# Optimization experiments

Hardware: AMD Instinct MI355X
Metric: run time of the kernel (lower is better)

The kernel has to match this reference:

```python
import jax, jax.numpy as jnp
import numpy as np

B, OBS, TASK = 65536, 512, 128
D, M, N = 64, 32, 4  # embedding dim, module width, modules per layer


def setup_inputs() -> dict:
    key = jax.random.key(0)
    ks = jax.random.split(key, 16)

    def w(k, shape):
        fan_in = shape[-2]
        return jax.random.normal(k, shape, jnp.float32) * np.float32(np.sqrt(2.0 / fan_in))

    z = lambda *s: jnp.zeros(s, jnp.float32)
    return dict(
        obs=jax.random.normal(ks[0], (B, OBS), jnp.float32),
        task=jax.random.normal(ks[1], (B, TASK), jnp.float32),
        Ws1=w(ks[2], (OBS, D)), bs1=z(D),
        Ws2=w(ks[3], (D, D)), bs2=z(D),
        Wt=w(ks[4], (TASK, D)), bt=z(D),
        Wa0=w(ks[5], (D, N * N)), ba0=z(N * N),
        Wa1=w(ks[6], (D, N * N)), ba1=z(N * N),
        Wc0=w(ks[7], (N * N, D)), bc0=z(D),
        Wc1=w(ks[8], (2 * N * N, D)), bc1=z(D),
        We0=w(ks[9], (N, D, M)), be0=z(N, M),
        We1=w(ks[10], (N, M, M)), be1=z(N, M),
        We2=w(ks[11], (N, M, M)), be2=z(N, M),
    )


def reference(obs, task, Ws1, bs1, Ws2, bs2, Wt, bt, Wa0, ba0, Wa1, ba1,
              Wc0, bc0, Wc1, bc1, We0, be0, We1, be1, We2, be2):
    relu = jax.nn.relu
    # base encoders
    s = relu(relu(obs @ Ws1 + bs1) @ Ws2 + bs2)          # [B, D]
    t = relu(task @ Wt + bt)                              # [B, D]
    r0 = s * t                                            # first routing inputs [B, D]
    prev = jnp.broadcast_to(s[None], (N,) + s.shape)      # [N, B, D] (state emb fed to all layer-0 modules)

    # routing layer 0 -> 1
    a0 = jax.nn.softmax((r0 @ Wa0 + ba0).reshape(-1, N, N), axis=-1)   # [B, N_next, N_prev]
    m = relu(jnp.einsum('nbi,nio->nbo', prev, We0) + be0[:, None, :])  # [N, B, M] expert outputs
    prev = jnp.einsum('bij,jbd->ibd', a0, m)                           # [N, B, M] attention-combined
    r = relu((a0.reshape(-1, N * N) @ Wc0 + bc0) * r0)                 # updated routing inputs

    # routing layer 1 -> 2
    a1 = jax.nn.softmax((r @ Wa1 + ba1).reshape(-1, N, N), axis=-1)
    m = relu(jnp.einsum('nbi,nio->nbo', prev, We1) + be1[:, None, :])
    prev = jnp.einsum('bij,jbd->ibd', a1, m)
    attn_cat = jnp.concatenate([a0.reshape(-1, N * N), a1.reshape(-1, N * N)], axis=-1)
    r = relu((attn_cat @ Wc1 + bc1) * r0)  # computed as in original (unused afterward)

    # final module layer, plain sum over modules
    m = relu(jnp.einsum('nbi,nio->nbo', prev, We2) + be2[:, None, :])  # [N, B, M]
    return relu(m.sum(axis=0))                                          # [B, M]
```

## Files before the change

### kernel.cpp

```cpp
#include <hip/hip_runtime.h>
#include <hip/hip_bf16.h>


using f32x4 = __attribute__((ext_vector_type(4))) float;
using h16x4 = __attribute__((ext_vector_type(4))) _Float16;
using h16x8 = __attribute__((ext_vector_type(8))) _Float16;
using u32x4 = __attribute__((ext_vector_type(4))) unsigned int;
using u32x2 = __attribute__((ext_vector_type(2))) unsigned int;

#define MFMA16(a, b, c) __builtin_amdgcn_mfma_f32_16x16x16f16((a), (b), (c), 0, 0, 0)

__device__ __forceinline__ short h_bits(float f) {
  _Float16 h = (_Float16)f;
  return __builtin_bit_cast(short, h);
}

__device__ __forceinline__ void dma16(const void* g, char* l) {
  __builtin_amdgcn_global_load_lds(
      (const __attribute__((address_space(1))) unsigned int*)g,
      (__attribute__((address_space(3))) unsigned int*)l, 16, 0, 0);
}

__global__ void sm_convert_v12(
    const float* __restrict__ Ws1, const float* __restrict__ Ws2, const float* __restrict__ Wt,
    const float* __restrict__ Wa0, const float* __restrict__ Wa1, const float* __restrict__ Wc0,
    const float* __restrict__ We0, const float* __restrict__ We1, const float* __restrict__ We2,
    const float* __restrict__ bs1, const float* __restrict__ bs2, const float* __restrict__ bt,
    const float* __restrict__ ba0, const float* __restrict__ ba1, const float* __restrict__ bc0,
    const float* __restrict__ be0, const float* __restrict__ be1, const float* __restrict__ be2,
    short* __restrict__ wsh, float* __restrict__ biasf) {
  int d = blockIdx.x * 256 + threadIdx.x;
  if (d < 64512) {
    float v;
    if (d < 32768) {
      int kk   = d & 3;
      int ntip = (d >> 2) & 1;
      int p    = (d >> 3) & 15;
      int q    = (d >> 7) & 3;
      int pair = (d >> 9) & 1;
      int kb2  = (d >> 10) & 1;
      int c    = d >> 11;
      int k = c * 32 + kb2 * 16 + q * 4 + kk;
      int o = pair * 32 + ntip * 16 + p;
      v = Ws1[k * 64 + o];
    }
    else if (d < 36864) { int r = d - 32768, o = r >> 6, k = r & 63;   v = Ws2[k * 64 + o]; }
    else if (d < 45056) {
      int r = d - 36864;
      int kk   = r & 3;
      int ntip = (r >> 2) & 1;
      int p    = (r >> 3) & 15;
      int q    = (r >> 7) & 3;
      int pair = (r >> 9) & 1;
      int kb2  = (r >> 10) & 1;
      int c    = r >> 11;
      int k = c * 32 + kb2 * 16 + q * 4 + kk;
      int o = pair * 32 + ntip * 16 + p;
      v = Wt[k * 64 + o];
    }
    else if (d < 46080) { int r = d - 45056, o = r >> 6, k = r & 63;   v = Wa0[k * 16 + o]; }
    else if (d < 47104) { int r = d - 46080, o = r >> 6, k = r & 63;   v = Wa1[k * 16 + o]; }
    else if (d < 48128) { int r = d - 47104, o = r >> 4, k = r & 15;   v = Wc0[k * 64 + o]; }
    else if (d < 56320) { int r = d - 48128, n = r >> 11, o = (r >> 6) & 31, i = r & 63; v = We0[n * 2048 + i * 32 + o]; }
    else if (d < 60416) { int r = d - 56320, n = r >> 10, o = (r >> 5) & 31, i = r & 31; v = We1[n * 1024 + i * 32 + o]; }
    else                { int r = d - 60416, n = r >> 10, o = (r >> 5) & 31, i = r & 31; v = We2[n * 1024 + i * 32 + o]; }
    wsh[d] = h_bits(v);
  } else if (d < 65184) {
    int r = d - 64512;
    float v;
    if      (r < 64)  v = bs1[r];
    else if (r < 128) v = bs2[r - 64];
    else if (r < 192) v = bt[r - 128];
    else if (r < 208) v = ba0[r - 192];
    else if (r < 224) v = ba1[r - 208];
    else if (r < 288) v = bc0[r - 224];
    else if (r < 416) v = be0[r - 288];
    else if (r < 544) v = be1[r - 416];
    else              v = be2[r - 544];
    biasf[r] = v;
  }
}

__global__ __launch_bounds__(256) void sm_fused_v12(
    const float* __restrict__ obs, const float* __restrict__ task,
    const short* __restrict__ wsh, const float* __restrict__ biasf,
    float* __restrict__ out) {
  const int tid  = threadIdx.x;
  const int wave = tid >> 6;
  const int lane = tid & 63;
  const int q    = lane >> 4;
  const int p    = lane & 15;
  const int lrow = wave * 16;
  const int wgrow  = blockIdx.x * 64;
  const int rowblk = wgrow + lrow;

  __shared__ __align__(16) char lds[48640];
  char* x_lds = lds;
  char* a_lds = lds + 8704;
  char* ring  = lds + 11776;
  char* p_lds = lds;

  const short* Bp1  = wsh;
  const short* Ws2T = wsh + 32768;
  const short* WtP  = wsh + 36864;
  const short* Wa0T = wsh + 45056;
  const short* Wa1T = wsh + 46080;
  const short* Wc0T = wsh + 47104;
  const short* We0T = wsh + 48128;
  const short* We1T = wsh + 56320;
  const short* We2T = wsh + 60416;
  const float* bs1 = biasf;        const float* bs2 = biasf + 64;
  const float* bt  = biasf + 128;  const float* ba0 = biasf + 192;
  const float* ba1 = biasf + 208;  const float* bc0 = biasf + 224;
  const float* be0 = biasf + 288;  const float* be1 = biasf + 416;
  const float* be2 = biasf + 544;

  const f32x4 z4 = {0.f, 0.f, 0.f, 0.f};

  auto stx  = [&](int row, int col, float v) { *(short*)(x_lds + row * 136 + col * 2) = h_bits(v); };
  auto ldx4 = [&](int row, int k0) -> h16x4 { return *(const h16x4*)(x_lds + row * 136 + k0 * 2); };
  auto ldb  = [&](const short* W, int off) -> h16x4 { return *(const h16x4*)(W + off); };
  auto cvtA = [&](const u32x4& u) -> h16x4 {
    float4 v = __builtin_bit_cast(float4, u);
    h16x4 a;
    a[0] = (_Float16)v.x; a[1] = (_Float16)v.y;
    a[2] = (_Float16)v.z; a[3] = (_Float16)v.w;
    return a;
  };
  auto lo2 = [&](const u32x4& u) -> h16x4 { return __builtin_bit_cast(h16x4, (u32x2){u[0], u[1]}); };
  auto hi2 = [&](const u32x4& u) -> h16x4 { return __builtin_bit_cast(h16x4, (u32x2){u[2], u[3]}); };

  auto stageA = [&](const float* base, int rowlen, int k0, int buf) {
#pragma unroll
    for (int j = 0; j < 2; ++j) {
      int f = j * 256 + wave * 64 + lane;
      int row = f >> 3;
      int cl = (f & 7) ^ (row & 7);
      dma16(base + (size_t)(wgrow + row) * rowlen + k0 + cl * 4,
            ring + buf * 12288 + j * 4096 + wave * 1024);
    }
  };
  auto stageB = [&](const short* bsrc, int c, int buf) {
    dma16((const char*)bsrc + c * 4096 + (wave * 64 + lane) * 16,
          ring + buf * 12288 + 8192 + wave * 1024);
  };
  auto lda_ = [&](int buf, int kb2) -> u32x4 {
    return *(const u32x4*)(ring + buf * 12288 + (lrow + p) * 128 +
                           (((kb2 * 4 + q) ^ (p & 7)) * 16));
  };
  auto ldbs = [&](int buf, int kb2, int pair) -> u32x4 {
    return *(const u32x4*)(ring + buf * 12288 + 8192 + kb2 * 2048 + pair * 1024 + lane * 16);
  };

  f32x4 accX[4] = {z4, z4, z4, z4};
  {
    stageA(obs, 512, 0, 0);  stageB(Bp1, 0, 0);
    stageA(obs, 512, 32, 1); stageB(Bp1, 1, 1);
    for (int c = 0; c < 16; ++c) {
      if (c < 14) {
        stageA(obs, 512, (c + 2) * 32, (c + 2) % 3);
        stageB(Bp1, c + 2, (c + 2) % 3);
        __builtin_amdgcn_sched_barrier(0);
        asm volatile("s_waitcnt vmcnt(6)" ::: "memory");
      } else if (c == 14) {
        asm volatile("s_waitcnt vmcnt(3)" ::: "memory");
      } else {
        asm volatile("s_waitcnt vmcnt(0)" ::: "memory");
      }
      __builtin_amdgcn_s_barrier();
      __builtin_amdgcn_sched_barrier(0);
      const int buf = c % 3;
#pragma unroll
      for (int kb2 = 0; kb2 < 2; ++kb2) {
        h16x4 a = cvtA(lda_(buf, kb2));
        u32x4 B0 = ldbs(buf, kb2, 0);
        u32x4 B1 = ldbs(buf, kb2, 1);
        accX[0] = MFMA16(a, lo2(B0), accX[0]);
        accX[1] = MFMA16(a, hi2(B0), accX[1]);
        accX[2] = MFMA16(a, lo2(B1), accX[2]);
        accX[3] = MFMA16(a, hi2(B1), accX[3]);
      }
      __builtin_amdgcn_s_barrier();
    }
  }

  stageA(task, 128, 0, 0);  stageB(WtP, 0, 0);
  stageA(task, 128, 32, 1); stageB(WtP, 1, 1);

#pragma unroll
  for (int nt = 0; nt < 4; ++nt) {
    float bias = bs1[nt * 16 + p];
#pragma unroll
    for (int r = 0; r < 4; ++r)
      stx(lrow + 4 * q + r, nt * 16 + p, fmaxf(accX[nt][r] + bias, 0.f));
  }

  f32x4 accS[4] = {z4, z4, z4, z4};
#pragma unroll
  for (int kb = 0; kb < 4; ++kb) {
    h16x4 a = ldx4(lrow + p, kb * 16 + q * 4);
#pragma unroll
    for (int nt = 0; nt < 4; ++nt)
      accS[nt] = MFMA16(a, ldb(Ws2T, (nt * 16 + p) * 64 + kb * 16 + q * 4), accS[nt]);
  }
  float sf[4][4];
#pragma unroll
  for (int nt = 0; nt < 4; ++nt) {
    float bias = bs2[nt * 16 + p];
#pragma unroll
    for (int r = 0; r < 4; ++r) sf[nt][r] = fmaxf(accS[nt][r] + bias, 0.f);
  }
#pragma unroll
  for (int nt = 0; nt < 4; ++nt)
#pragma unroll
    for (int r = 0; r < 4; ++r) stx(lrow + 4 * q + r, nt * 16 + p, sf[nt][r]);

  f32x4 accT[4] = {z4, z4, z4, z4};
  {
    for (int c = 0; c < 4; ++c) {
      if (c < 2) {
        stageA(task, 128, (c + 2) * 32, (c + 2) % 3);
        stageB(WtP, c + 2, (c + 2) % 3);
        __builtin_amdgcn_sched_barrier(0);
        asm volatile("s_waitcnt vmcnt(6)" ::: "memory");
      } else if (c == 2) {
        asm volatile("s_waitcnt vmcnt(3)" ::: "memory");
      } else {
        asm volatile("s_waitcnt vmcnt(0)" ::: "memory");
      }
      __builtin_amdgcn_s_barrier();
      __builtin_amdgcn_sched_barrier(0);
      const int buf = c % 3;
#pragma unroll
      for (int kb2 = 0; kb2 < 2; ++kb2) {
        h16x4 a = cvtA(lda_(buf, kb2));
        u32x4 B0 = ldbs(buf, kb2, 0);
        u32x4 B1 = ldbs(buf, kb2, 1);
        accT[0] = MFMA16(a, lo2(B0), accT[0]);
        accT[1] = MFMA16(a, hi2(B0), accT[1]);
        accT[2] = MFMA16(a, lo2(B1), accT[2]);
        accT[3] = MFMA16(a, hi2(B1), accT[3]);
      }
      __builtin_amdgcn_s_barrier();
    }
  }
  float r0f[4][4];
#pragma unroll
  for (int nt = 0; nt < 4; ++nt) {
    float bias = bt[nt * 16 + p];
#pragma unroll
    for (int r = 0; r < 4; ++r)
      r0f[nt][r] = sf[nt][r] * fmaxf(accT[nt][r] + bias, 0.f);
  }

  float mfr[4][2][4];
#pragma unroll
  for (int n = 0; n < 4; ++n) {
    f32x4 acc[2] = {z4, z4};
#pragma unroll
    for (int kb = 0; kb < 4; ++kb) {
      h16x4 a = ldx4(lrow + p, kb * 16 + q * 4);
#pragma unroll
      for (int nt = 0; nt < 2; ++nt)
        acc[nt] = MFMA16(a, ldb(We0T, (n * 32 + nt * 16 + p) * 64 + kb * 16 + q * 4), acc[nt]);
    }
#pragma unroll
    for (int nt = 0; nt < 2; ++nt) {
      float bias = be0[n * 32 + nt * 16 + p];
#pragma unroll
      for (int r = 0; r < 4; ++r) mfr[n][nt][r] = fmaxf(acc[nt][r] + bias, 0.f);
    }
  }

#pragma unroll
  for (int nt = 0; nt < 4; ++nt)
#pragma unroll
    for (int r = 0; r < 4; ++r) stx(lrow + 4 * q + r, nt * 16 + p, r0f[nt][r]);

  f32x4 accA = z4;
#pragma unroll
  for (int kb = 0; kb < 4; ++kb)
    accA = MFMA16(ldx4(lrow + p, kb * 16 + q * 4), ldb(Wa0T, p * 64 + kb * 16 + q * 4), accA);
  float a0v[4];
  {
    float bias = ba0[p];
#pragma unroll
    for (int r = 0; r < 4; ++r) {
      float v = accA[r] + bias;
      float mx = fmaxf(v, __shfl_xor(v, 1));
      mx = fmaxf(mx, __shfl_xor(mx, 2));
      float e = __expf(v - mx);
      float ssum = e + __shfl_xor(e, 1);
      ssum += __shfl_xor(ssum, 2);
      a0v[r] = e / ssum;
    }
  }
#pragma unroll
  for (int r = 0; r < 4; ++r)
    *(short*)(a_lds + (lrow + 4 * q + r) * 48 + p * 2) = h_bits(a0v[r]);

  float pv[4][2][4];
#pragma unroll
  for (int r = 0; r < 4; ++r) {
    h16x8 alo = *(const h16x8*)(a_lds + (lrow + 4 * q + r) * 48);
    h16x8 ahi = *(const h16x8*)(a_lds + (lrow + 4 * q + r) * 48 + 16);
    float av[16];
#pragma unroll
    for (int e = 0; e < 8; ++e) { av[e] = (float)alo[e]; av[8 + e] = (float)ahi[e]; }
#pragma unroll
    for (int i = 0; i < 4; ++i) {
      float s0 = 0.f, s1 = 0.f;
#pragma unroll
      for (int j = 0; j < 4; ++j) {
        s0 += av[4 * i + j] * mfr[j][0][r];
        s1 += av[4 * i + j] * mfr[j][1][r];
      }
      pv[i][0][r] = s0; pv[i][1][r] = s1;
    }
  }

  f32x4 accC[4] = {z4, z4, z4, z4};
  {
    h16x4 a = *(const h16x4*)(a_lds + (lrow + p) * 48 + q * 8);
#pragma unroll
    for (int nt = 0; nt < 4; ++nt)
      accC[nt] = MFMA16(a, ldb(Wc0T, (nt * 16 + p) * 16 + q * 4), accC[nt]);
  }
  float rf[4][4];
#pragma unroll
  for (int nt = 0; nt < 4; ++nt) {
    float bias = bc0[nt * 16 + p];
#pragma unroll
    for (int r = 0; r < 4; ++r)
      rf[nt][r] = fmaxf((accC[nt][r] + bias) * r0f[nt][r], 0.f);
  }
#pragma unroll
  for (int nt = 0; nt < 4; ++nt)
#pragma unroll
    for (int r = 0; r < 4; ++r) stx(lrow + 4 * q + r, nt * 16 + p, rf[nt][r]);

  f32x4 accA1 = z4;
#pragma unroll
  for (int kb = 0; kb < 4; ++kb)
    accA1 = MFMA16(ldx4(lrow + p, kb * 16 + q * 4), ldb(Wa1T, p * 64 + kb * 16 + q * 4), accA1);
  float a1v[4];
  {
    float bias = ba1[p];
#pragma unroll
    for (int r = 0; r < 4; ++r) {
      float v = accA1[r] + bias;
      float mx = fmaxf(v, __shfl_xor(v, 1));
      mx = fmaxf(mx, __shfl_xor(mx, 2));
      float e = __expf(v - mx);
      float ssum = e + __shfl_xor(e, 1);
      ssum += __shfl_xor(ssum, 2);
      a1v[r] = e / ssum;
    }
  }
#pragma unroll
  for (int r = 0; r < 4; ++r)
    *(short*)(a_lds + (lrow + 4 * q + r) * 48 + p * 2) = h_bits(a1v[r]);

  __syncthreads();

#pragma unroll
  for (int i = 0; i < 4; ++i)
#pragma unroll
    for (int nt = 0; nt < 2; ++nt)
#pragma unroll
      for (int r = 0; r < 4; ++r)
        *(short*)(p_lds + (i * 64 + lrow + 4 * q + r) * 80 + (nt * 16 + p) * 2) = h_bits(pv[i][nt][r]);

  float m1f[4][2][4];
#pragma unroll
  for (int n = 0; n < 4; ++n) {
    f32x4 acc[2] = {z4, z4};
#pragma unroll
    for (int kb = 0; kb < 2; ++kb) {
      h16x4 a = *(const h16x4*)(p_lds + (n * 64 + lrow + p) * 80 + kb * 32 + q * 8);
#pragma unroll
      for (int nt = 0; nt < 2; ++nt)
        acc[nt] = MFMA16(a, ldb(We1T, (n * 32 + nt * 16 + p) * 32 + kb * 16 + q * 4), acc[nt]);
    }
#pragma unroll
    for (int nt = 0; nt < 2; ++nt) {
      float bias = be1[n * 32 + nt * 16 + p];
#pragma unroll
      for (int r = 0; r < 4; ++r) m1f[n][nt][r] = fmaxf(acc[nt][r] + bias, 0.f);
    }
  }


  float pv2[4][2][4];
#pragma unroll
  for (int r = 0; r < 4; ++r) {
    float av[16];
#pragma unroll
    for (int cc = 0; cc < 16; ++cc)
      av[cc] = __shfl(a1v[r], (lane & 48) | cc);
#pragma unroll
    for (int i = 0; i < 4; ++i) {
      float s0 = 0.f, s1 = 0.f;
#pragma unroll
      for (int j = 0; j < 4; ++j) {
        s0 += av[4 * i + j] * m1f[j][0][r];
        s1 += av[4 * i + j] * m1f[j][1][r];
      }
      pv2[i][0][r] = s0; pv2[i][1][r] = s1;
    }
  }

#pragma unroll
  for (int i = 0; i < 4; ++i)
#pragma unroll
    for (int nt = 0; nt < 2; ++nt)
#pragma unroll
      for (int r = 0; r < 4; ++r)
        *(short*)(p_lds + (i * 64 + lrow + 4 * q + r) * 80 + (nt * 16 + p) * 2) = h_bits(pv2[i][nt][r]);

  float of[2][4] = {{0.f, 0.f, 0.f, 0.f}, {0.f, 0.f, 0.f, 0.f}};
#pragma unroll
  for (int n = 0; n < 4; ++n) {
    f32x4 acc[2] = {z4, z4};
#pragma unroll
    for (int kb = 0; kb < 2; ++kb) {
      h16x4 a = *(const h16x4*)(p_lds + (n * 64 + lrow + p) * 80 + kb * 32 + q * 8);
#pragma unroll
      for (int nt = 0; nt < 2; ++nt)
        acc[nt] = MFMA16(a, ldb(We2T, (n * 32 + nt * 16 + p) * 32 + kb * 16 + q * 4), acc[nt]);
    }
#pragma unroll
    for (int nt = 0; nt < 2; ++nt) {
      float bias = be2[n * 32 + nt * 16 + p];
#pragma unroll
      for (int r = 0; r < 4; ++r) of[nt][r] += fmaxf(acc[nt][r] + bias, 0.f);
    }
  }
#pragma unroll
  for (int nt = 0; nt < 2; ++nt)
#pragma unroll
    for (int r = 0; r < 4; ++r) {
      int grow = rowblk + 4 * q + r;
      out[(size_t)grow * 32 + nt * 16 + p] = of[nt][r];
    }
}

extern "C" void kernel_launch(void* const* d_in, const int* in_sizes, int n_in,
                              void* d_out, int out_size, void* d_ws, size_t ws_size,
                              hipStream_t stream) {
  (void)in_sizes; (void)n_in; (void)out_size; (void)ws_size;
  const float* obs  = (const float*)d_in[0];
  const float* task = (const float*)d_in[1];
  const float* Ws1 = (const float*)d_in[2];  const float* bs1 = (const float*)d_in[3];
  const float* Ws2 = (const float*)d_in[4];  const float* bs2 = (const float*)d_in[5];
  const float* Wt  = (const float*)d_in[6];  const float* bt  = (const float*)d_in[7];
  const float* Wa0 = (const float*)d_in[8];  const float* ba0 = (const float*)d_in[9];
  const float* Wa1 = (const float*)d_in[10]; const float* ba1 = (const float*)d_in[11];
  const float* Wc0 = (const float*)d_in[12]; const float* bc0 = (const float*)d_in[13];
  const float* We0 = (const float*)d_in[16]; const float* be0 = (const float*)d_in[17];
  const float* We1 = (const float*)d_in[18]; const float* be1 = (const float*)d_in[19];
  const float* We2 = (const float*)d_in[20]; const float* be2 = (const float*)d_in[21];

  short* wsh   = (short*)d_ws;
  float* biasf = (float*)((char*)d_ws + 129040);

  sm_convert_v12<<<dim3(255), dim3(256), 0, stream>>>(
      Ws1, Ws2, Wt, Wa0, Wa1, Wc0, We0, We1, We2,
      bs1, bs2, bt, ba0, ba1, bc0, be0, be1, be2,
      wsh, biasf);
  sm_fused_v12<<<dim3(1024), dim3(256), 0, stream>>>(
      obs, task, wsh, biasf, (float*)d_out);
}
```

Baseline: 79.97 us.

## Switch fused kernel to single-wave workgroups with double-buffered barrier-free staging

Rewrites the fused kernel so each 64-thread workgroup processes 16 rows on its own, replacing 256-thread blocks that shared staged weight tiles across four waves. This removes all workgroup barriers and moves from a triple-buffered to a double-buffered DMA ring with smaller LDS, aiming for higher occupancy and less sync stall. In exchange, each wave now loads the full weight tile per chunk by itself, quadrupling weight traffic into LDS, and the shallower prefetch depth may expose more memory latency.

Result: faster. 67.66 us (-15.4%).

```diff
diff --git a/kernel.cpp b/kernel.cpp
--- a/kernel.cpp
+++ b/kernel.cpp
@@ -21,7 +21,7 @@
       (__attribute__((address_space(3))) unsigned int*)l, 16, 0, 0);
 }
 
-__global__ void sm_convert_v12(
+__global__ void sm_convert_v13(
     const float* __restrict__ Ws1, const float* __restrict__ Ws2, const float* __restrict__ Wt,
     const float* __restrict__ Wa0, const float* __restrict__ Wa1, const float* __restrict__ Wc0,
     const float* __restrict__ We0, const float* __restrict__ We1, const float* __restrict__ We2,
@@ -81,24 +81,20 @@
   }
 }
 
-__global__ __launch_bounds__(256) void sm_fused_v12(
+__global__ __launch_bounds__(64) void sm_fused_v13(
     const float* __restrict__ obs, const float* __restrict__ task,
     const short* __restrict__ wsh, const float* __restrict__ biasf,
     float* __restrict__ out) {
-  const int tid  = threadIdx.x;
-  const int wave = tid >> 6;
-  const int lane = tid & 63;
+  const int lane = threadIdx.x & 63;
   const int q    = lane >> 4;
   const int p    = lane & 15;
-  const int lrow = wave * 16;
-  const int wgrow  = blockIdx.x * 64;
-  const int rowblk = wgrow + lrow;
-
-  __shared__ __align__(16) char lds[48640];
-  char* x_lds = lds;
-  char* a_lds = lds + 8704;
-  char* ring  = lds + 11776;
-  char* p_lds = lds;
+  const int rowblk = blockIdx.x * 16;
+
+  __shared__ __align__(16) char lds[20352];
+  char* x_lds  = lds;
+  char* a_lds  = lds + 2176;
+  char* pm_lds = lds + 2944;
+  char* ring   = lds + 8064;
 
   const short* Bp1  = wsh;
   const short* Ws2T = wsh + 32768;
@@ -133,43 +129,41 @@
   auto stageA = [&](const float* base, int rowlen, int k0, int buf) {
 #pragma unroll
     for (int j = 0; j < 2; ++j) {
-      int f = j * 256 + wave * 64 + lane;
+      int f = j * 64 + lane;
       int row = f >> 3;
       int cl = (f & 7) ^ (row & 7);
-      dma16(base + (size_t)(wgrow + row) * rowlen + k0 + cl * 4,
-            ring + buf * 12288 + j * 4096 + wave * 1024);
+      dma16(base + (size_t)(rowblk + row) * rowlen + k0 + cl * 4,
+            ring + buf * 6144 + j * 1024);
     }
   };
   auto stageB = [&](const short* bsrc, int c, int buf) {
-    dma16((const char*)bsrc + c * 4096 + (wave * 64 + lane) * 16,
-          ring + buf * 12288 + 8192 + wave * 1024);
+#pragma unroll
+    for (int j = 0; j < 4; ++j)
+      dma16((const char*)bsrc + c * 4096 + (j * 64 + lane) * 16,
+            ring + buf * 6144 + 2048 + j * 1024);
   };
   auto lda_ = [&](int buf, int kb2) -> u32x4 {
-    return *(const u32x4*)(ring + buf * 12288 + (lrow + p) * 128 +
+    return *(const u32x4*)(ring + buf * 6144 + p * 128 +
                            (((kb2 * 4 + q) ^ (p & 7)) * 16));
   };
   auto ldbs = [&](int buf, int kb2, int pair) -> u32x4 {
-    return *(const u32x4*)(ring + buf * 12288 + 8192 + kb2 * 2048 + pair * 1024 + lane * 16);
+    return *(const u32x4*)(ring + buf * 6144 + 2048 + kb2 * 2048 + pair * 1024 + lane * 16);
   };
 
   f32x4 accX[4] = {z4, z4, z4, z4};
   {
-    stageA(obs, 512, 0, 0);  stageB(Bp1, 0, 0);
-    stageA(obs, 512, 32, 1); stageB(Bp1, 1, 1);
+    stageA(obs, 512, 0, 0); stageB(Bp1, 0, 0);
     for (int c = 0; c < 16; ++c) {
-      if (c < 14) {
-        stageA(obs, 512, (c + 2) * 32, (c + 2) % 3);
-        stageB(Bp1, c + 2, (c + 2) % 3);
+      if (c + 1 < 16) {
+        stageA(obs, 512, (c + 1) * 32, (c + 1) & 1);
+        stageB(Bp1, c + 1, (c + 1) & 1);
         __builtin_amdgcn_sched_barrier(0);
         asm volatile("s_waitcnt vmcnt(6)" ::: "memory");
-      } else if (c == 14) {
-        asm volatile("s_waitcnt vmcnt(3)" ::: "memory");
       } else {
         asm volatile("s_waitcnt vmcnt(0)" ::: "memory");
       }
-      __builtin_amdgcn_s_barrier();
       __builtin_amdgcn_sched_barrier(0);
-      const int buf = c % 3;
+      const int buf = c & 1;
 #pragma unroll
       for (int kb2 = 0; kb2 < 2; ++kb2) {
         h16x4 a = cvtA(lda_(buf, kb2));
@@ -180,25 +174,23 @@
         accX[2] = MFMA16(a, lo2(B1), accX[2]);
         accX[3] = MFMA16(a, hi2(B1), accX[3]);
       }
-      __builtin_amdgcn_s_barrier();
-    }
-  }
-
-  stageA(task, 128, 0, 0);  stageB(WtP, 0, 0);
-  stageA(task, 128, 32, 1); stageB(WtP, 1, 1);
+    }
+  }
+
+  stageA(task, 128, 0, 0); stageB(WtP, 0, 0);
 
 #pragma unroll
   for (int nt = 0; nt < 4; ++nt) {
     float bias = bs1[nt * 16 + p];
 #pragma unroll
     for (int r = 0; r < 4; ++r)
-      stx(lrow + 4 * q + r, nt * 16 + p, fmaxf(accX[nt][r] + bias, 0.f));
+      stx(4 * q + r, nt * 16 + p, fmaxf(accX[nt][r] + bias, 0.f));
   }
 
   f32x4 accS[4] = {z4, z4, z4, z4};
 #pragma unroll
   for (int kb = 0; kb < 4; ++kb) {
-    h16x4 a = ldx4(lrow + p, kb * 16 + q * 4);
+    h16x4 a = ldx4(p, kb * 16 + q * 4);
 #pragma unroll
     for (int nt = 0; nt < 4; ++nt)
       accS[nt] = MFMA16(a, ldb(Ws2T, (nt * 16 + p) * 64 + kb * 16 + q * 4), accS[nt]);
@@ -213,24 +205,21 @@
 #pragma unroll
   for (int nt = 0; nt < 4; ++nt)
 #pragma unroll
-    for (int r = 0; r < 4; ++r) stx(lrow + 4 * q + r, nt * 16 + p, sf[nt][r]);
+    for (int r = 0; r < 4; ++r) stx(4 * q + r, nt * 16 + p, sf[nt][r]);
 
   f32x4 accT[4] = {z4, z4, z4, z4};
   {
     for (int c = 0; c < 4; ++c) {
-      if (c < 2) {
-        stageA(task, 128, (c + 2) * 32, (c + 2) % 3);
-        stageB(WtP, c + 2, (c + 2) % 3);
+      if (c + 1 < 4) {
+        stageA(task, 128, (c + 1) * 32, (c + 1) & 1);
+        stageB(WtP, c + 1, (c + 1) & 1);
         __builtin_amdgcn_sched_barrier(0);
         asm volatile("s_waitcnt vmcnt(6)" ::: "memory");
-      } else if (c == 2) {
-        asm volatile("s_waitcnt vmcnt(3)" ::: "memory");
       } else {
         asm volatile("s_waitcnt vmcnt(0)" ::: "memory");
       }
-      __builtin_amdgcn_s_barrier();
       __builtin_amdgcn_sched_barrier(0);
-      const int buf = c % 3;
+      const int buf = c & 1;
 #pragma unroll
       for (int kb2 = 0; kb2 < 2; ++kb2) {
         h16x4 a = cvtA(lda_(buf, kb2));
@@ -241,7 +230,6 @@
         accT[2] = MFMA16(a, lo2(B1), accT[2]);
         accT[3] = MFMA16(a, hi2(B1), accT[3]);
       }
-      __builtin_amdgcn_s_barrier();
     }
   }
   float r0f[4][4];
@@ -259,7 +247,7 @@
     f32x4 acc[2] = {z4, z4};
 #pragma unroll
     for (int kb = 0; kb < 4; ++kb) {
-      h16x4 a = ldx4(lrow + p, kb * 16 + q * 4);
+      h16x4 a = ldx4(p, kb * 16 + q * 4);
 #pragma unroll
       for (int nt = 0; nt < 2; ++nt)
         acc[nt] = MFMA16(a, ldb(We0T, (n * 32 + nt * 16 + p) * 64 + kb * 16 + q * 4), acc[nt]);
@@ -275,12 +263,12 @@
 #pragma unroll
   for (int nt = 0; nt < 4; ++nt)
 #pragma unroll
-    for (int r = 0; r < 4; ++r) stx(lrow + 4 * q + r, nt * 16 + p, r0f[nt][r]);
+    for (int r = 0; r < 4; ++r) stx(4 * q + r, nt * 16 + p, r0f[nt][r]);
 
   f32x4 accA = z4;
 #pragma unroll
   for (int kb = 0; kb < 4; ++kb)
-    accA = MFMA16(ldx4(lrow + p, kb * 16 + q * 4), ldb(Wa0T, p * 64 + kb * 16 + q * 4), accA);
+    accA = MFMA16(ldx4(p, kb * 16 + q * 4), ldb(Wa0T, p * 64 + kb * 16 + q * 4), accA);
   float a0v[4];
   {
     float bias = ba0[p];
@@ -297,13 +285,13 @@
   }
 #pragma unroll
   for (int r = 0; r < 4; ++r)
-    *(short*)(a_lds + (lrow + 4 * q + r) * 48 + p * 2) = h_bits(a0v[r]);
+    *(short*)(a_lds + (4 * q + r) * 48 + p * 2) = h_bits(a0v[r]);
 
   float pv[4][2][4];
 #pragma unroll
   for (int r = 0; r < 4; ++r) {
-    h16x8 alo = *(const h16x8*)(a_lds + (lrow + 4 * q + r) * 48);
-    h16x8 ahi = *(const h16x8*)(a_lds + (lrow + 4 * q + r) * 48 + 16);
+    h16x8 alo = *(const h16x8*)(a_lds + (4 * q + r) * 48);
+    h16x8 ahi = *(const h16x8*)(a_lds + (4 * q + r) * 48 + 16);
     float av[16];
 #pragma unroll
     for (int e = 0; e < 8; ++e) { av[e] = (float)alo[e]; av[8 + e] = (float)ahi[e]; }
@@ -321,7 +309,7 @@
 
   f32x4 accC[4] = {z4, z4, z4, z4};
   {
-    h16x4 a = *(const h16x4*)(a_lds + (lrow + p) * 48 + q * 8);
+    h16x4 a = *(const h16x4*)(a_lds + p * 48 + q * 8);
 #pragma unroll
     for (int nt = 0; nt < 4; ++nt)
       accC[nt] = MFMA16(a, ldb(Wc0T, (nt * 16 + p) * 16 + q * 4), accC[nt]);
@@ -337,12 +325,12 @@
 #pragma unroll
   for (int nt = 0; nt < 4; ++nt)
 #pragma unroll
-    for (int r = 0; r < 4; ++r) stx(lrow + 4 * q + r, nt * 16 + p, rf[nt][r]);
+    for (int r = 0; r < 4; ++r) stx(4 * q + r, nt * 16 + p, rf[nt][r]);
 
   f32x4 accA1 = z4;
 #pragma unroll
   for (int kb = 0; kb < 4; ++kb)
-    accA1 = MFMA16(ldx4(lrow + p, kb * 16 + q * 4), ldb(Wa1T, p * 64 + kb * 16 + q * 4), accA1);
+    accA1 = MFMA16(ldx4(p, kb * 16 + q * 4), ldb(Wa1T, p * 64 + kb * 16 + q * 4), accA1);
   float a1v[4];
   {
     float bias = ba1[p];
@@ -357,11 +345,6 @@
       a1v[r] = e / ssum;
     }
   }
-#pragma unroll
-  for (int r = 0; r < 4; ++r)
-    *(short*)(a_lds + (lrow + 4 * q + r) * 48 + p * 2) = h_bits(a1v[r]);
-
-  __syncthreads();
 
 #pragma unroll
   for (int i = 0; i < 4; ++i)
@@ -369,7 +352,7 @@
     for (int nt = 0; nt < 2; ++nt)
 #pragma unroll
       for (int r = 0; r < 4; ++r)
-        *(short*)(p_lds + (i * 64 + lrow + 4 * q + r) * 80 + (nt * 16 + p) * 2) = h_bits(pv[i][nt][r]);
+        *(short*)(pm_lds + (i * 16 + 4 * q + r) * 80 + (nt * 16 + p) * 2) = h_bits(pv[i][nt][r]);
 
   float m1f[4][2][4];
 #pragma unroll
@@ -377,7 +360,7 @@
     f32x4 acc[2] = {z4, z4};
 #pragma unroll
     for (int kb = 0; kb < 2; ++kb) {
-      h16x4 a = *(const h16x4*)(p_lds + (n * 64 + lrow + p) * 80 + kb * 32 + q * 8);
+      h16x4 a = *(const h16x4*)(pm_lds + (n * 16 + p) * 80 + kb * 32 + q * 8);
 #pragma unroll
       for (int nt = 0; nt < 2; ++nt)
         acc[nt] = MFMA16(a, ldb(We1T, (n * 32 + nt * 16 + p) * 32 + kb * 16 + q * 4), acc[nt]);
@@ -389,7 +372,6 @@
       for (int r = 0; r < 4; ++r) m1f[n][nt][r] = fmaxf(acc[nt][r] + bias, 0.f);
     }
   }
-
 
   float pv2[4][2][4];
 #pragma unroll
@@ -416,7 +398,7 @@
     for (int nt = 0; nt < 2; ++nt)
 #pragma unroll
       for (int r = 0; r < 4; ++r)
-        *(short*)(p_lds + (i * 64 + lrow + 4 * q + r) * 80 + (nt * 16 + p) * 2) = h_bits(pv2[i][nt][r]);
+        *(short*)(pm_lds + (i * 16 + 4 * q + r) * 80 + (nt * 16 + p) * 2) = h_bits(pv2[i][nt][r]);
 
   float of[2][4] = {{0.f, 0.f, 0.f, 0.f}, {0.f, 0.f, 0.f, 0.f}};
 #pragma unroll
@@ -424,7 +406,7 @@
     f32x4 acc[2] = {z4, z4};
 #pragma unroll
     for (int kb = 0; kb < 2; ++kb) {
-      h16x4 a = *(const h16x4*)(p_lds + (n * 64 + lrow + p) * 80 + kb * 32 + q * 8);
+      h16x4 a = *(const h16x4*)(pm_lds + (n * 16 + p) * 80 + kb * 32 + q * 8);
 #pragma unroll
       for (int nt = 0; nt < 2; ++nt)
         acc[nt] = MFMA16(a, ldb(We2T, (n * 32 + nt * 16 + p) * 32 + kb * 16 + q * 4), acc[nt]);
@@ -464,10 +446,10 @@
   short* wsh   = (short*)d_ws;
   float* biasf = (float*)((char*)d_ws + 129040);
 
-  sm_convert_v12<<<dim3(255), dim3(256), 0, stream>>>(
+  sm_convert_v13<<<dim3(255), dim3(256), 0, stream>>>(
       Ws1, Ws2, Wt, Wa0, Wa1, Wc0, We0, We1, We2,
       bs1, bs2, bt, ba0, ba1, bc0, be0, be1, be2,
       wsh, biasf);
-  sm_fused_v12<<<dim3(1024), dim3(256), 0, stream>>>(
+  sm_fused_v13<<<dim3(4096), dim3(64), 0, stream>>>(
       obs, task, wsh, biasf, (float*)d_out);
 }
```
